# Optimization experiments

Measured on AMD Instinct MI355X. Metric: run time of the kernel, lower is better.

Reference implementation:

```python
import jax, jax.numpy as jnp
import numpy as np

B, T, E, H = 8, 2048, 1024, 64

def setup_inputs() -> dict:
    key = jax.random.key(0)
    kx, kq, kk, kv = jax.random.split(key, 4)
    x = jax.random.normal(kx, (B, T, E), dtype=jnp.float32)
    # torch Linear(E, H, bias=False): weight [H, E]; store transposed [E, H]
    scale = 1.0 / np.sqrt(E)
    Wq = jax.random.uniform(kq, (E, H), dtype=jnp.float32, minval=-scale, maxval=scale)
    Wk = jax.random.uniform(kk, (E, H), dtype=jnp.float32, minval=-scale, maxval=scale)
    Wv = jax.random.uniform(kv, (E, H), dtype=jnp.float32, minval=-scale, maxval=scale)
    return {"x": x, "Wq": Wq, "Wk": Wk, "Wv": Wv}

def reference(x, Wq, Wk, Wv):
    # x: [B,T,E]
    q = x @ Wq  # [B,T,H]
    k = x @ Wk
    v = x @ Wv
    head_size = q.shape[-1]
    scores = jnp.einsum('bth,bsh->bts', q, k) * (head_size ** -0.5)  # [B,T,T]
    Tlen = x.shape[1]
    causal = jnp.tril(jnp.ones((Tlen, Tlen), dtype=bool))
    scores = jnp.where(causal, scores, -jnp.inf)
    weights = jax.nn.softmax(scores, axis=-1)
    # dropout p=0.0 -> identity
    out = jnp.einsum('bts,bsh->bth', weights, v)  # [B,T,H]
    return out
```

## Files before the change

kernel.cpp:

```cpp
#include <hip/hip_runtime.h>
#include <hip/hip_bf16.h>

#define B_  8
#define T_  2048
#define E_  1024
#define H_  64
#define BT_ (B_*T_)

typedef __attribute__((ext_vector_type(8))) __bf16 bf16x8;
typedef __attribute__((ext_vector_type(4))) float  f32x4;

__device__ __forceinline__ unsigned short f2bfu(float f) {
    union { float f; unsigned u; } v; v.f = f;
    unsigned r = v.u + 0x7fffu + ((v.u >> 16) & 1u);
    return (unsigned short)(r >> 16);
}

__device__ __forceinline__ unsigned pk2(float lo, float hi) {
    __hip_bfloat162 h = __float22bfloat162_rn(float2{lo, hi});
    union { __hip_bfloat162 h; unsigned u; } v; v.h = h;
    return v.u;
}

#if defined(__has_builtin)
#if __has_builtin(__builtin_amdgcn_global_load_lds)
#define HAVE_GLL 1
#endif
#endif
__device__ __forceinline__ void dma16(const void* g, void* lds_base, int lane) {
#ifdef HAVE_GLL
    __builtin_amdgcn_global_load_lds(
        (const __attribute__((address_space(1))) unsigned*)(unsigned long long)g,
        (__attribute__((address_space(3))) unsigned*)(unsigned)(unsigned long long)lds_base,
        16, 0, 0);
#else
    *(uint4*)((char*)lds_base + lane * 16) = *(const uint4*)g;
#endif
}

#define QSCALE (0.125f * 1.44269504f)

#define WF_CHUNK_BYTES 12288

__global__ __launch_bounds__(256)
void wprep_kernel(const float* __restrict__ Wq,
                  const float* __restrict__ Wk,
                  const float* __restrict__ Wv,
                  unsigned short* __restrict__ wf)
{
    const int c = blockIdx.x / 3;
    const int m = blockIdx.x % 3;
    const float* W = (m == 0) ? Wq : (m == 1 ? Wk : Wv);
    const float scale = (m == 0) ? QSCALE : 1.0f;

    const int n    = threadIdx.x >> 6;
    const int lane = threadIdx.x & 63;
    const int quad = lane >> 4;
    const int col  = lane & 15;
    const int h    = n * 16 + col;

    unsigned short tmp[8];
#pragma unroll
    for (int j = 0; j < 8; ++j)
        tmp[j] = f2bfu(W[(c * 32 + quad * 8 + j) * H_ + h] * scale);
    *(uint4*)&wf[(((c * 3 + m) * 4 + n) * 64 + lane) * 8] = *(uint4*)tmp;
}

__global__ __launch_bounds__(256, 4)
void qkv_kernel(const float* __restrict__ x,
                const unsigned short* __restrict__ wf,
                unsigned short* __restrict__ qb,
                unsigned short* __restrict__ kb,
                unsigned short* __restrict__ vtb)
{
    __shared__ __align__(16) char  wfs[2][WF_CHUNK_BYTES];
    __shared__ __align__(16) float xs[2][512];

    const int tid  = threadIdx.x;
    const int w    = tid >> 6;
    const int lane = tid & 63;
    const int quad = lane >> 4;
    const int col  = lane & 15;
    const long r0  = (long)blockIdx.x * 16;

    f32x4 acc[3];
#pragma unroll
    for (int m = 0; m < 3; ++m) acc[m] = (f32x4){0.f, 0.f, 0.f, 0.f};

    const char* wfb = (const char*)wf;

    const float* xg = x + (r0 + w * 8 + (lane >> 3)) * E_ + (((lane & 7) ^ (lane >> 3)) * 4);

    const int s0 = (2 * quad) ^ (col & 7);
    const int s1 = s0 ^ 1;

#pragma unroll
    for (int j = 0; j < 3; ++j)
        dma16(wfb + (w * 3 + j) * 1024 + lane * 16, &wfs[0][(w * 3 + j) * 1024], lane);
    if (w < 2) dma16(xg, &xs[0][w * 256], lane);

    for (int c = 0; c < 32; ++c) {
        const int buf = c & 1;
        __syncthreads();

        if (c + 1 < 32) {
#pragma unroll
            for (int j = 0; j < 3; ++j)
                dma16(wfb + (long)(c + 1) * WF_CHUNK_BYTES + (w * 3 + j) * 1024 + lane * 16,
                      &wfs[buf ^ 1][(w * 3 + j) * 1024], lane);
            if (w < 2) dma16(xg + (c + 1) * 32, &xs[buf ^ 1][w * 256], lane);
        }

        float4 f0 = *(const float4*)&xs[buf][col * 32 + s0 * 4];
        float4 f1 = *(const float4*)&xs[buf][col * 32 + s1 * 4];
        unsigned pk[4];
        pk[0] = pk2(f0.x, f0.y);
        pk[1] = pk2(f0.z, f0.w);
        pk[2] = pk2(f1.x, f1.y);
        pk[3] = pk2(f1.z, f1.w);
        bf16x8 af = *(bf16x8*)pk;

#pragma unroll
        for (int m = 0; m < 3; ++m) {
            bf16x8 bm = *(const bf16x8*)&wfs[buf][m * 4096 + w * 1024 + lane * 16];
            acc[m] = __builtin_amdgcn_mfma_f32_16x16x32_bf16(af, bm, acc[m], 0, 0, 0);
        }
    }

    const int bidx = (int)(r0 >> 11);
    const int h    = w * 16 + col;
#pragma unroll
    for (int r = 0; r < 4; ++r) {
        long t = r0 + quad * 4 + r;
        qb[t * H_ + h] = f2bfu(acc[0][r]);
        kb[t * H_ + h] = f2bfu(acc[1][r]);
        vtb[((long)(bidx * H_ + h)) * T_ + (t & (T_ - 1))] = f2bfu(acc[2][r]);
    }
}

#define PSS 72

__global__ __launch_bounds__(512, 2)
void attn_kernel(const unsigned short* __restrict__ qb,
                 const unsigned short* __restrict__ kb,
                 const unsigned short* __restrict__ vtb,
                 float* __restrict__ out)
{
    __shared__ char smem[8 * 16 * 68 * 4 + 8 * 2 * 16 * 4];
    unsigned short* ps = (unsigned short*)smem;
    float* oc = (float*)smem;
    float* ml = (float*)(smem + 8 * 16 * 68 * 4);

    const int tid  = threadIdx.x;
    const int g    = tid >> 6;
    const int lane = tid & 63;
    const int quad = lane >> 4;
    const int col  = lane & 15;
    const int b    = blockIdx.x & 7;
    const int p    = blockIdx.x >> 3;

    const unsigned short* qbb = qb  + (long)b * T_ * H_;
    const unsigned short* kbb = kb  + (long)b * T_ * H_;
    const unsigned short* vbb = vtb + (long)b * H_ * T_;

    for (int half = 0; half < 2; ++half) {
        const int qt = half ? (127 - p) : p;
        const int nt = (qt + 4) >> 2;

        bf16x8 qa0 = *(const bf16x8*)&qbb[(qt * 16 + col) * H_ + quad * 8];
        bf16x8 qa1 = *(const bf16x8*)&qbb[(qt * 16 + col) * H_ + 32 + quad * 8];

        f32x4 o[4];
        float m_i[4], l_i[4];
#pragma unroll
        for (int n = 0; n < 4; ++n) o[n] = (f32x4){0.f, 0.f, 0.f, 0.f};
#pragma unroll
        for (int r = 0; r < 4; ++r) { m_i[r] = -1e30f; l_i[r] = 0.f; }

        bf16x8 kf[8];
        if (g < nt) {
#pragma unroll
            for (int kt = 0; kt < 4; ++kt) {
                const unsigned short* kp = kbb + ((long)(g * 64 + kt * 16 + col)) * H_ + quad * 8;
                kf[kt * 2]     = *(const bf16x8*)kp;
                kf[kt * 2 + 1] = *(const bf16x8*)(kp + 32);
            }
        }

        for (int s = g; s < nt; s += 8) {
            f32x4 sa[4];
#pragma unroll
            for (int kt = 0; kt < 4; ++kt) {
                sa[kt] = (f32x4){0.f, 0.f, 0.f, 0.f};
                sa[kt] = __builtin_amdgcn_mfma_f32_16x16x32_bf16(qa0, kf[kt * 2],     sa[kt], 0, 0, 0);
                sa[kt] = __builtin_amdgcn_mfma_f32_16x16x32_bf16(qa1, kf[kt * 2 + 1], sa[kt], 0, 0, 0);
            }

            bf16x8 vf[8];
#pragma unroll
            for (int n = 0; n < 4; ++n) {
                const unsigned short* vp = vbb + ((long)(n * 16 + col)) * T_ + s * 64 + quad * 8;
                vf[n * 2]     = *(const bf16x8*)vp;
                vf[n * 2 + 1] = *(const bf16x8*)(vp + 32);
            }

            if (s + 8 < nt) {
#pragma unroll
                for (int kt = 0; kt < 4; ++kt) {
                    const unsigned short* kp = kbb + ((long)((s + 8) * 64 + kt * 16 + col)) * H_ + quad * 8;
                    kf[kt * 2]     = *(const bf16x8*)kp;
                    kf[kt * 2 + 1] = *(const bf16x8*)(kp + 32);
                }
            }

            if (s == nt - 1) {
#pragma unroll
                for (int kt = 0; kt < 4; ++kt) {
                    int kg = s * 64 + kt * 16 + col;
#pragma unroll
                    for (int r = 0; r < 4; ++r) {
                        int qg = qt * 16 + quad * 4 + r;
                        if (kg > qg) sa[kt][r] = -1e30f;
                    }
                }
            }

            float mx[4];
#pragma unroll
            for (int r = 0; r < 4; ++r)
                mx[r] = fmaxf(fmaxf(sa[0][r], sa[1][r]), fmaxf(sa[2][r], sa[3][r]));
#pragma unroll
            for (int off = 1; off < 16; off <<= 1)
#pragma unroll
                for (int r = 0; r < 4; ++r)
                    mx[r] = fmaxf(mx[r], __shfl_xor(mx[r], off, 64));

            float alpha[4], mnew[4];
#pragma unroll
            for (int r = 0; r < 4; ++r) {
                mnew[r]  = fmaxf(m_i[r], mx[r]);
                alpha[r] = __builtin_amdgcn_exp2f(m_i[r] - mnew[r]);
                m_i[r]   = mnew[r];
            }

            float rs[4] = {0.f, 0.f, 0.f, 0.f};
#pragma unroll
            for (int kt = 0; kt < 4; ++kt)
#pragma unroll
                for (int r = 0; r < 4; ++r) {
                    float pv = __builtin_amdgcn_exp2f(sa[kt][r] - mnew[r]);
                    rs[r] += pv;
                    ps[g * 16 * PSS + (quad * 4 + r) * PSS + kt * 16 + col] = f2bfu(pv);
                }
#pragma unroll
            for (int off = 1; off < 16; off <<= 1)
#pragma unroll
                for (int r = 0; r < 4; ++r)
                    rs[r] += __shfl_xor(rs[r], off, 64);
#pragma unroll
            for (int r = 0; r < 4; ++r)
                l_i[r] = l_i[r] * alpha[r] + rs[r];

#pragma unroll
            for (int n = 0; n < 4; ++n)
#pragma unroll
                for (int r = 0; r < 4; ++r)
                    o[n][r] *= alpha[r];

            bf16x8 pa0 = *(const bf16x8*)&ps[g * 16 * PSS + col * PSS + quad * 8];
            bf16x8 pa1 = *(const bf16x8*)&ps[g * 16 * PSS + col * PSS + 32 + quad * 8];
#pragma unroll
            for (int n = 0; n < 4; ++n) {
                o[n] = __builtin_amdgcn_mfma_f32_16x16x32_bf16(pa0, vf[n * 2],     o[n], 0, 0, 0);
                o[n] = __builtin_amdgcn_mfma_f32_16x16x32_bf16(pa1, vf[n * 2 + 1], o[n], 0, 0, 0);
            }
        }

        __syncthreads();
#pragma unroll
        for (int r = 0; r < 4; ++r) {
            int row = quad * 4 + r;
#pragma unroll
            for (int n = 0; n < 4; ++n)
                oc[(g * 16 + row) * 68 + n * 16 + col] = o[n][r];
        }
        if (col == 0) {
#pragma unroll
            for (int r = 0; r < 4; ++r) {
                ml[(g * 2 + 0) * 16 + quad * 4 + r] = m_i[r];
                ml[(g * 2 + 1) * 16 + quad * 4 + r] = l_i[r];
            }
        }
        __syncthreads();

#pragma unroll
        for (int rr = 0; rr < 2; ++rr) {
            int row = g * 2 + rr;
            float M = ml[0 * 32 + row];
#pragma unroll
            for (int j = 1; j < 8; ++j) M = fmaxf(M, ml[j * 32 + row]);
            float lsum = 0.f, osum = 0.f;
#pragma unroll
            for (int j = 0; j < 8; ++j) {
                float wgt = __builtin_amdgcn_exp2f(ml[j * 32 + row] - M);
                lsum += ml[j * 32 + 16 + row] * wgt;
                osum += oc[(j * 16 + row) * 68 + lane] * wgt;
            }
            out[((long)b * T_ + qt * 16 + row) * H_ + lane] = osum / lsum;
        }
        __syncthreads();
    }
}

extern "C" void kernel_launch(void* const* d_in, const int* in_sizes, int n_in,
                              void* d_out, int out_size, void* d_ws, size_t ws_size,
                              hipStream_t stream) {
    (void)in_sizes; (void)n_in; (void)out_size; (void)ws_size;
    const float* x  = (const float*)d_in[0];
    const float* Wq = (const float*)d_in[1];
    const float* Wk = (const float*)d_in[2];
    const float* Wv = (const float*)d_in[3];

    unsigned short* qb  = (unsigned short*)d_ws;
    unsigned short* kb  = qb + (size_t)BT_ * H_;
    unsigned short* vtb = kb + (size_t)BT_ * H_;
    unsigned short* wf  = vtb + (size_t)BT_ * H_;

    wprep_kernel<<<96, 256, 0, stream>>>(Wq, Wk, Wv, wf);
    qkv_kernel<<<BT_ / 16, 256, 0, stream>>>(x, wf, qb, kb, vtb);
    attn_kernel<<<B_ * 64, 512, 0, stream>>>(qb, kb, vtb, (float*)d_out);
}
```

Before: 159.8 us.

## Fuse weight prep, QKV projection and attention into one persistent kernel

Replaces three kernel launches with a single persistent kernel of 256 blocks that runs the weight repack, the QKV projection and causal attention in sequence. The phases are separated by software grid barriers built on atomic counters, which are reset with a memset before launch. This removes launch gaps and kernel boundaries. In exchange the grid shrinks from 1024 and 512 blocks to 256 blocks that each do multiple work units, which lowers parallelism and load balancing. The barriers also rely on all blocks being co-resident and add their own spin-wait cost.

Result: slower. 259.4 us (+62.3%).

```diff
diff --git a/kernel.cpp b/kernel.cpp
--- a/kernel.cpp
+++ b/kernel.cpp
@@ -6,6 +6,7 @@
 #define E_  1024
 #define H_  64
 #define BT_ (B_*T_)
+#define NBLK 256
 
 typedef __attribute__((ext_vector_type(8))) __bf16 bf16x8;
 typedef __attribute__((ext_vector_type(4))) float  f32x4;
@@ -38,277 +39,297 @@
 #endif
 }
 
+__device__ __forceinline__ void gridbar(unsigned* cnt, unsigned expected) {
+    __syncthreads();
+    if (threadIdx.x == 0) {
+        __threadfence();
+        __hip_atomic_fetch_add(cnt, 1u, __ATOMIC_RELEASE, __HIP_MEMORY_SCOPE_AGENT);
+        while (__hip_atomic_load(cnt, __ATOMIC_ACQUIRE, __HIP_MEMORY_SCOPE_AGENT) < expected)
+            __builtin_amdgcn_s_sleep(2);
+        __threadfence();
+    }
+    __syncthreads();
+}
+
 #define QSCALE (0.125f * 1.44269504f)
-
 #define WF_CHUNK_BYTES 12288
-
-__global__ __launch_bounds__(256)
-void wprep_kernel(const float* __restrict__ Wq,
+#define PSS 72
+
+__global__ __launch_bounds__(512, 2)
+void fused_kernel(const float* __restrict__ x,
+                  const float* __restrict__ Wq,
                   const float* __restrict__ Wk,
                   const float* __restrict__ Wv,
-                  unsigned short* __restrict__ wf)
+                  unsigned short* __restrict__ qb,
+                  unsigned short* __restrict__ kb,
+                  unsigned short* __restrict__ vtb,
+                  unsigned short* __restrict__ wf,
+                  float* __restrict__ out,
+                  unsigned* __restrict__ bar)
 {
-    const int c = blockIdx.x / 3;
-    const int m = blockIdx.x % 3;
-    const float* W = (m == 0) ? Wq : (m == 1 ? Wk : Wv);
-    const float scale = (m == 0) ? QSCALE : 1.0f;
-
-    const int n    = threadIdx.x >> 6;
-    const int lane = threadIdx.x & 63;
-    const int quad = lane >> 4;
-    const int col  = lane & 15;
-    const int h    = n * 16 + col;
-
-    unsigned short tmp[8];
-#pragma unroll
-    for (int j = 0; j < 8; ++j)
-        tmp[j] = f2bfu(W[(c * 32 + quad * 8 + j) * H_ + h] * scale);
-    *(uint4*)&wf[(((c * 3 + m) * 4 + n) * 64 + lane) * 8] = *(uint4*)tmp;
-}
-
-__global__ __launch_bounds__(256, 4)
-void qkv_kernel(const float* __restrict__ x,
-                const unsigned short* __restrict__ wf,
-                unsigned short* __restrict__ qb,
-                unsigned short* __restrict__ kb,
-                unsigned short* __restrict__ vtb)
-{
-    __shared__ __align__(16) char  wfs[2][WF_CHUNK_BYTES];
-    __shared__ __align__(16) float xs[2][512];
-
-    const int tid  = threadIdx.x;
-    const int w    = tid >> 6;
-    const int lane = tid & 63;
-    const int quad = lane >> 4;
-    const int col  = lane & 15;
-    const long r0  = (long)blockIdx.x * 16;
-
-    f32x4 acc[3];
-#pragma unroll
-    for (int m = 0; m < 3; ++m) acc[m] = (f32x4){0.f, 0.f, 0.f, 0.f};
-
-    const char* wfb = (const char*)wf;
-
-    const float* xg = x + (r0 + w * 8 + (lane >> 3)) * E_ + (((lane & 7) ^ (lane >> 3)) * 4);
-
-    const int s0 = (2 * quad) ^ (col & 7);
-    const int s1 = s0 ^ 1;
-
-#pragma unroll
-    for (int j = 0; j < 3; ++j)
-        dma16(wfb + (w * 3 + j) * 1024 + lane * 16, &wfs[0][(w * 3 + j) * 1024], lane);
-    if (w < 2) dma16(xg, &xs[0][w * 256], lane);
-
-    for (int c = 0; c < 32; ++c) {
-        const int buf = c & 1;
-        __syncthreads();
-
-        if (c + 1 < 32) {
-#pragma unroll
-            for (int j = 0; j < 3; ++j)
-                dma16(wfb + (long)(c + 1) * WF_CHUNK_BYTES + (w * 3 + j) * 1024 + lane * 16,
-                      &wfs[buf ^ 1][(w * 3 + j) * 1024], lane);
-            if (w < 2) dma16(xg + (c + 1) * 32, &xs[buf ^ 1][w * 256], lane);
-        }
-
-        float4 f0 = *(const float4*)&xs[buf][col * 32 + s0 * 4];
-        float4 f1 = *(const float4*)&xs[buf][col * 32 + s1 * 4];
-        unsigned pk[4];
-        pk[0] = pk2(f0.x, f0.y);
-        pk[1] = pk2(f0.z, f0.w);
-        pk[2] = pk2(f1.x, f1.y);
-        pk[3] = pk2(f1.z, f1.w);
-        bf16x8 af = *(bf16x8*)pk;
-
-#pragma unroll
-        for (int m = 0; m < 3; ++m) {
-            bf16x8 bm = *(const bf16x8*)&wfs[buf][m * 4096 + w * 1024 + lane * 16];
-            acc[m] = __builtin_amdgcn_mfma_f32_16x16x32_bf16(af, bm, acc[m], 0, 0, 0);
+    __shared__ __align__(16) char smem[35840];
+    const int tid = threadIdx.x;
+
+    {
+        const int t = blockIdx.x * 512 + tid;
+        if (t < 96 * 256) {
+            const int vb = t >> 8;
+            const int vt = t & 255;
+            const int c = vb / 3;
+            const int m = vb % 3;
+            const float* W = (m == 0) ? Wq : (m == 1 ? Wk : Wv);
+            const float scale = (m == 0) ? QSCALE : 1.0f;
+            const int n    = vt >> 6;
+            const int lane = vt & 63;
+            const int quad = lane >> 4;
+            const int col  = lane & 15;
+            const int h    = n * 16 + col;
+            unsigned short tmp[8];
+#pragma unroll
+            for (int j = 0; j < 8; ++j)
+                tmp[j] = f2bfu(W[(c * 32 + quad * 8 + j) * H_ + h] * scale);
+            *(uint4*)&wf[(((c * 3 + m) * 4 + n) * 64 + lane) * 8] = *(uint4*)tmp;
         }
     }
-
-    const int bidx = (int)(r0 >> 11);
-    const int h    = w * 16 + col;
-#pragma unroll
-    for (int r = 0; r < 4; ++r) {
-        long t = r0 + quad * 4 + r;
-        qb[t * H_ + h] = f2bfu(acc[0][r]);
-        kb[t * H_ + h] = f2bfu(acc[1][r]);
-        vtb[((long)(bidx * H_ + h)) * T_ + (t & (T_ - 1))] = f2bfu(acc[2][r]);
-    }
-}
-
-#define PSS 72
-
-__global__ __launch_bounds__(512, 2)
-void attn_kernel(const unsigned short* __restrict__ qb,
-                 const unsigned short* __restrict__ kb,
-                 const unsigned short* __restrict__ vtb,
-                 float* __restrict__ out)
-{
-    __shared__ char smem[8 * 16 * 68 * 4 + 8 * 2 * 16 * 4];
-    unsigned short* ps = (unsigned short*)smem;
-    float* oc = (float*)smem;
-    float* ml = (float*)(smem + 8 * 16 * 68 * 4);
-
-    const int tid  = threadIdx.x;
-    const int g    = tid >> 6;
-    const int lane = tid & 63;
-    const int quad = lane >> 4;
-    const int col  = lane & 15;
-    const int b    = blockIdx.x & 7;
-    const int p    = blockIdx.x >> 3;
-
-    const unsigned short* qbb = qb  + (long)b * T_ * H_;
-    const unsigned short* kbb = kb  + (long)b * T_ * H_;
-    const unsigned short* vbb = vtb + (long)b * H_ * T_;
-
-    for (int half = 0; half < 2; ++half) {
-        const int qt = half ? (127 - p) : p;
-        const int nt = (qt + 4) >> 2;
-
-        bf16x8 qa0 = *(const bf16x8*)&qbb[(qt * 16 + col) * H_ + quad * 8];
-        bf16x8 qa1 = *(const bf16x8*)&qbb[(qt * 16 + col) * H_ + 32 + quad * 8];
-
-        f32x4 o[4];
-        float m_i[4], l_i[4];
-#pragma unroll
-        for (int n = 0; n < 4; ++n) o[n] = (f32x4){0.f, 0.f, 0.f, 0.f};
-#pragma unroll
-        for (int r = 0; r < 4; ++r) { m_i[r] = -1e30f; l_i[r] = 0.f; }
-
-        bf16x8 kf[8];
-        if (g < nt) {
-#pragma unroll
-            for (int kt = 0; kt < 4; ++kt) {
-                const unsigned short* kp = kbb + ((long)(g * 64 + kt * 16 + col)) * H_ + quad * 8;
-                kf[kt * 2]     = *(const bf16x8*)kp;
-                kf[kt * 2 + 1] = *(const bf16x8*)(kp + 32);
+    gridbar(&bar[0], NBLK);
+
+    {
+        char*  wfs = smem;
+        float* xsb = (float*)(smem + 24576);
+        const int w8   = tid >> 6;
+        const int a    = w8 >> 2;
+        const int wa   = w8 & 3;
+        const int lane = tid & 63;
+        const int quad = lane >> 4;
+        const int col  = lane & 15;
+        const char* wfb = (const char*)wf;
+        const int s0 = (2 * quad) ^ (col & 7);
+        const int s1 = s0 ^ 1;
+        float* xs = xsb + a * 1024;
+
+        for (int pass = 0; pass < 2; ++pass) {
+            const long r0 = ((long)blockIdx.x * 2 + a + pass * 512) * 16;
+            const float* xg = x + (r0 + wa * 8 + (lane >> 3)) * E_
+                                + (((lane & 7) ^ (lane >> 3)) * 4);
+
+            f32x4 acc[3];
+#pragma unroll
+            for (int m = 0; m < 3; ++m) acc[m] = (f32x4){0.f, 0.f, 0.f, 0.f};
+
+            dma16(wfb + w8 * 1024 + lane * 16, &wfs[w8 * 1024], lane);
+            if (w8 < 4)
+                dma16(wfb + (8 + w8) * 1024 + lane * 16, &wfs[(8 + w8) * 1024], lane);
+            if (wa < 2) dma16(xg, &xs[wa * 256], lane);
+
+            for (int c = 0; c < 32; ++c) {
+                const int buf = c & 1;
+                __syncthreads();
+
+                if (c + 1 < 32) {
+                    const char* src = wfb + (long)(c + 1) * WF_CHUNK_BYTES;
+                    char* dst = &wfs[(buf ^ 1) * 12288];
+                    dma16(src + w8 * 1024 + lane * 16, dst + w8 * 1024, lane);
+                    if (w8 < 4)
+                        dma16(src + (8 + w8) * 1024 + lane * 16, dst + (8 + w8) * 1024, lane);
+                    if (wa < 2) dma16(xg + (c + 1) * 32, &xs[(buf ^ 1) * 512 + wa * 256], lane);
+                }
+
+                float4 f0 = *(const float4*)&xs[buf * 512 + col * 32 + s0 * 4];
+                float4 f1 = *(const float4*)&xs[buf * 512 + col * 32 + s1 * 4];
+                unsigned pk[4];
+                pk[0] = pk2(f0.x, f0.y);
+                pk[1] = pk2(f0.z, f0.w);
+                pk[2] = pk2(f1.x, f1.y);
+                pk[3] = pk2(f1.z, f1.w);
+                bf16x8 af = *(bf16x8*)pk;
+
+#pragma unroll
+                for (int m = 0; m < 3; ++m) {
+                    bf16x8 bm = *(const bf16x8*)&wfs[buf * 12288 + m * 4096 + wa * 1024 + lane * 16];
+                    acc[m] = __builtin_amdgcn_mfma_f32_16x16x32_bf16(af, bm, acc[m], 0, 0, 0);
+                }
+            }
+
+            const int bidx = (int)(r0 >> 11);
+            const int h    = wa * 16 + col;
+#pragma unroll
+            for (int r = 0; r < 4; ++r) {
+                long t = r0 + quad * 4 + r;
+                qb[t * H_ + h] = f2bfu(acc[0][r]);
+                kb[t * H_ + h] = f2bfu(acc[1][r]);
+                vtb[((long)(bidx * H_ + h)) * T_ + (t & (T_ - 1))] = f2bfu(acc[2][r]);
             }
         }
-
-        for (int s = g; s < nt; s += 8) {
-            f32x4 sa[4];
-#pragma unroll
-            for (int kt = 0; kt < 4; ++kt) {
-                sa[kt] = (f32x4){0.f, 0.f, 0.f, 0.f};
-                sa[kt] = __builtin_amdgcn_mfma_f32_16x16x32_bf16(qa0, kf[kt * 2],     sa[kt], 0, 0, 0);
-                sa[kt] = __builtin_amdgcn_mfma_f32_16x16x32_bf16(qa1, kf[kt * 2 + 1], sa[kt], 0, 0, 0);
-            }
-
-            bf16x8 vf[8];
-#pragma unroll
-            for (int n = 0; n < 4; ++n) {
-                const unsigned short* vp = vbb + ((long)(n * 16 + col)) * T_ + s * 64 + quad * 8;
-                vf[n * 2]     = *(const bf16x8*)vp;
-                vf[n * 2 + 1] = *(const bf16x8*)(vp + 32);
-            }
-
-            if (s + 8 < nt) {
-#pragma unroll
-                for (int kt = 0; kt < 4; ++kt) {
-                    const unsigned short* kp = kbb + ((long)((s + 8) * 64 + kt * 16 + col)) * H_ + quad * 8;
-                    kf[kt * 2]     = *(const bf16x8*)kp;
-                    kf[kt * 2 + 1] = *(const bf16x8*)(kp + 32);
-                }
-            }
-
-            if (s == nt - 1) {
-#pragma unroll
-                for (int kt = 0; kt < 4; ++kt) {
-                    int kg = s * 64 + kt * 16 + col;
+    }
+    gridbar(&bar[1], NBLK);
+
+    {
+        unsigned short* ps = (unsigned short*)smem;
+        float* oc = (float*)smem;
+        float* ml = (float*)(smem + 8 * 16 * 68 * 4);
+
+        const int g    = tid >> 6;
+        const int lane = tid & 63;
+        const int quad = lane >> 4;
+        const int col  = lane & 15;
+
+        for (int u = 0; u < 2; ++u) {
+            const int unit = blockIdx.x + u * NBLK;
+            const int b = unit & 7;
+            const int p = unit >> 3;
+
+            const unsigned short* qbb = qb  + (long)b * T_ * H_;
+            const unsigned short* kbb = kb  + (long)b * T_ * H_;
+            const unsigned short* vbb = vtb + (long)b * H_ * T_;
+
+            for (int half = 0; half < 2; ++half) {
+                const int qt = half ? (127 - p) : p;
+                const int nt = (qt + 4) >> 2;
+
+                bf16x8 qa0 = *(const bf16x8*)&qbb[(qt * 16 + col) * H_ + quad * 8];
+                bf16x8 qa1 = *(const bf16x8*)&qbb[(qt * 16 + col) * H_ + 32 + quad * 8];
+
+                f32x4 o[4];
+                float m_i[4], l_i[4];
+#pragma unroll
+                for (int n = 0; n < 4; ++n) o[n] = (f32x4){0.f, 0.f, 0.f, 0.f};
+#pragma unroll
+                for (int r = 0; r < 4; ++r) { m_i[r] = -1e30f; l_i[r] = 0.f; }
+
+                bf16x8 kf[8];
+                if (g < nt) {
+#pragma unroll
+                    for (int kt = 0; kt < 4; ++kt) {
+                        const unsigned short* kp = kbb + ((long)(g * 64 + kt * 16 + col)) * H_ + quad * 8;
+                        kf[kt * 2]     = *(const bf16x8*)kp;
+                        kf[kt * 2 + 1] = *(const bf16x8*)(kp + 32);
+                    }
+                }
+
+                for (int s = g; s < nt; s += 8) {
+                    f32x4 sa[4];
+#pragma unroll
+                    for (int kt = 0; kt < 4; ++kt) {
+                        sa[kt] = (f32x4){0.f, 0.f, 0.f, 0.f};
+                        sa[kt] = __builtin_amdgcn_mfma_f32_16x16x32_bf16(qa0, kf[kt * 2],     sa[kt], 0, 0, 0);
+                        sa[kt] = __builtin_amdgcn_mfma_f32_16x16x32_bf16(qa1, kf[kt * 2 + 1], sa[kt], 0, 0, 0);
+                    }
+
+                    bf16x8 vf[8];
+#pragma unroll
+                    for (int n = 0; n < 4; ++n) {
+                        const unsigned short* vp = vbb + ((long)(n * 16 + col)) * T_ + s * 64 + quad * 8;
+                        vf[n * 2]     = *(const bf16x8*)vp;
+                        vf[n * 2 + 1] = *(const bf16x8*)(vp + 32);
+                    }
+
+                    if (s + 8 < nt) {
+#pragma unroll
+                        for (int kt = 0; kt < 4; ++kt) {
+                            const unsigned short* kp = kbb + ((long)((s + 8) * 64 + kt * 16 + col)) * H_ + quad * 8;
+                            kf[kt * 2]     = *(const bf16x8*)kp;
+                            kf[kt * 2 + 1] = *(const bf16x8*)(kp + 32);
+                        }
+                    }
+
+                    if (s == nt - 1) {
+#pragma unroll
+                        for (int kt = 0; kt < 4; ++kt) {
+                            int kg = s * 64 + kt * 16 + col;
+#pragma unroll
+                            for (int r = 0; r < 4; ++r) {
+                                int qg = qt * 16 + quad * 4 + r;
+                                if (kg > qg) sa[kt][r] = -1e30f;
+                            }
+                        }
+                    }
+
+                    float mx[4];
+#pragma unroll
+                    for (int r = 0; r < 4; ++r)
+                        mx[r] = fmaxf(fmaxf(sa[0][r], sa[1][r]), fmaxf(sa[2][r], sa[3][r]));
+#pragma unroll
+                    for (int off = 1; off < 16; off <<= 1)
+#pragma unroll
+                        for (int r = 0; r < 4; ++r)
+                            mx[r] = fmaxf(mx[r], __shfl_xor(mx[r], off, 64));
+
+                    float alpha[4], mnew[4];
 #pragma unroll
                     for (int r = 0; r < 4; ++r) {
-                        int qg = qt * 16 + quad * 4 + r;
-                        if (kg > qg) sa[kt][r] = -1e30f;
-                    }
-                }
-            }
-
-            float mx[4];
-#pragma unroll
-            for (int r = 0; r < 4; ++r)
-                mx[r] = fmaxf(fmaxf(sa[0][r], sa[1][r]), fmaxf(sa[2][r], sa[3][r]));
-#pragma unroll
-            for (int off = 1; off < 16; off <<= 1)
-#pragma unroll
-                for (int r = 0; r < 4; ++r)
-                    mx[r] = fmaxf(mx[r], __shfl_xor(mx[r], off, 64));
-
-            float alpha[4], mnew[4];
-#pragma unroll
-            for (int r = 0; r < 4; ++r) {
-                mnew[r]  = fmaxf(m_i[r], mx[r]);
-                alpha[r] = __builtin_amdgcn_exp2f(m_i[r] - mnew[r]);
-                m_i[r]   = mnew[r];
-            }
-
-            float rs[4] = {0.f, 0.f, 0.f, 0.f};
-#pragma unroll
-            for (int kt = 0; kt < 4; ++kt)
+                        mnew[r]  = fmaxf(m_i[r], mx[r]);
+                        alpha[r] = __builtin_amdgcn_exp2f(m_i[r] - mnew[r]);
+                        m_i[r]   = mnew[r];
+                    }
+
+                    float rs[4] = {0.f, 0.f, 0.f, 0.f};
+#pragma unroll
+                    for (int kt = 0; kt < 4; ++kt)
+#pragma unroll
+                        for (int r = 0; r < 4; ++r) {
+                            float pv = __builtin_amdgcn_exp2f(sa[kt][r] - mnew[r]);
+                            rs[r] += pv;
+                            ps[g * 16 * PSS + (quad * 4 + r) * PSS + kt * 16 + col] = f2bfu(pv);
+                        }
+#pragma unroll
+                    for (int off = 1; off < 16; off <<= 1)
+#pragma unroll
+                        for (int r = 0; r < 4; ++r)
+                            rs[r] += __shfl_xor(rs[r], off, 64);
+#pragma unroll
+                    for (int r = 0; r < 4; ++r)
+                        l_i[r] = l_i[r] * alpha[r] + rs[r];
+
+#pragma unroll
+                    for (int n = 0; n < 4; ++n)
+#pragma unroll
+                        for (int r = 0; r < 4; ++r)
+                            o[n][r] *= alpha[r];
+
+                    bf16x8 pa0 = *(const bf16x8*)&ps[g * 16 * PSS + col * PSS + quad * 8];
+                    bf16x8 pa1 = *(const bf16x8*)&ps[g * 16 * PSS + col * PSS + 32 + quad * 8];
+#pragma unroll
+                    for (int n = 0; n < 4; ++n) {
+                        o[n] = __builtin_amdgcn_mfma_f32_16x16x32_bf16(pa0, vf[n * 2],     o[n], 0, 0, 0);
+                        o[n] = __builtin_amdgcn_mfma_f32_16x16x32_bf16(pa1, vf[n * 2 + 1], o[n], 0, 0, 0);
+                    }
+                }
+
+                __syncthreads();
 #pragma unroll
                 for (int r = 0; r < 4; ++r) {
-                    float pv = __builtin_amdgcn_exp2f(sa[kt][r] - mnew[r]);
-                    rs[r] += pv;
-                    ps[g * 16 * PSS + (quad * 4 + r) * PSS + kt * 16 + col] = f2bfu(pv);
-                }
-#pragma unroll
-            for (int off = 1; off < 16; off <<= 1)
-#pragma unroll
-                for (int r = 0; r < 4; ++r)
-                    rs[r] += __shfl_xor(rs[r], off, 64);
-#pragma unroll
-            for (int r = 0; r < 4; ++r)
-                l_i[r] = l_i[r] * alpha[r] + rs[r];
-
-#pragma unroll
-            for (int n = 0; n < 4; ++n)
-#pragma unroll
-                for (int r = 0; r < 4; ++r)
-                    o[n][r] *= alpha[r];
-
-            bf16x8 pa0 = *(const bf16x8*)&ps[g * 16 * PSS + col * PSS + quad * 8];
-            bf16x8 pa1 = *(const bf16x8*)&ps[g * 16 * PSS + col * PSS + 32 + quad * 8];
-#pragma unroll
-            for (int n = 0; n < 4; ++n) {
-                o[n] = __builtin_amdgcn_mfma_f32_16x16x32_bf16(pa0, vf[n * 2],     o[n], 0, 0, 0);
-                o[n] = __builtin_amdgcn_mfma_f32_16x16x32_bf16(pa1, vf[n * 2 + 1], o[n], 0, 0, 0);
+                    int row = quad * 4 + r;
+#pragma unroll
+                    for (int n = 0; n < 4; ++n)
+                        oc[(g * 16 + row) * 68 + n * 16 + col] = o[n][r];
+                }
+                if (col == 0) {
+#pragma unroll
+                    for (int r = 0; r < 4; ++r) {
+                        ml[(g * 2 + 0) * 16 + quad * 4 + r] = m_i[r];
+                        ml[(g * 2 + 1) * 16 + quad * 4 + r] = l_i[r];
+                    }
+                }
+                __syncthreads();
+
+#pragma unroll
+                for (int rr = 0; rr < 2; ++rr) {
+                    int row = g * 2 + rr;
+                    float M = ml[0 * 32 + row];
+#pragma unroll
+                    for (int j = 1; j < 8; ++j) M = fmaxf(M, ml[j * 32 + row]);
+                    float lsum = 0.f, osum = 0.f;
+#pragma unroll
+                    for (int j = 0; j < 8; ++j) {
+                        float wgt = __builtin_amdgcn_exp2f(ml[j * 32 + row] - M);
+                        lsum += ml[j * 32 + 16 + row] * wgt;
+                        osum += oc[(j * 16 + row) * 68 + lane] * wgt;
+                    }
+                    out[((long)b * T_ + qt * 16 + row) * H_ + lane] = osum / lsum;
+                }
+                __syncthreads();
             }
         }
-
-        __syncthreads();
-#pragma unroll
-        for (int r = 0; r < 4; ++r) {
-            int row = quad * 4 + r;
-#pragma unroll
-            for (int n = 0; n < 4; ++n)
-                oc[(g * 16 + row) * 68 + n * 16 + col] = o[n][r];
-        }
-        if (col == 0) {
-#pragma unroll
-            for (int r = 0; r < 4; ++r) {
-                ml[(g * 2 + 0) * 16 + quad * 4 + r] = m_i[r];
-                ml[(g * 2 + 1) * 16 + quad * 4 + r] = l_i[r];
-            }
-        }
-        __syncthreads();
-
-#pragma unroll
-        for (int rr = 0; rr < 2; ++rr) {
-            int row = g * 2 + rr;
-            float M = ml[0 * 32 + row];
-#pragma unroll
-            for (int j = 1; j < 8; ++j) M = fmaxf(M, ml[j * 32 + row]);
-            float lsum = 0.f, osum = 0.f;
-#pragma unroll
-            for (int j = 0; j < 8; ++j) {
-                float wgt = __builtin_amdgcn_exp2f(ml[j * 32 + row] - M);
-                lsum += ml[j * 32 + 16 + row] * wgt;
-                osum += oc[(j * 16 + row) * 68 + lane] * wgt;
-            }
-            out[((long)b * T_ + qt * 16 + row) * H_ + lane] = osum / lsum;
-        }
-        __syncthreads();
     }
 }
 
@@ -325,8 +346,9 @@
     unsigned short* kb  = qb + (size_t)BT_ * H_;
     unsigned short* vtb = kb + (size_t)BT_ * H_;
     unsigned short* wf  = vtb + (size_t)BT_ * H_;
-
-    wprep_kernel<<<96, 256, 0, stream>>>(Wq, Wk, Wv, wf);
-    qkv_kernel<<<BT_ / 16, 256, 0, stream>>>(x, wf, qb, kb, vtb);
-    attn_kernel<<<B_ * 64, 512, 0, stream>>>(qb, kb, vtb, (float*)d_out);
-}
+    unsigned*       bar = (unsigned*)(wf + (size_t)3 * H_ * E_);
+    float*          out = (float*)d_out;
+
+    hipMemsetAsync(bar, 0, 64, stream);
+    fused_kernel<<<NBLK, 512, 0, stream>>>(x, Wq, Wk, Wv, qb, kb, vtb, wf, out, bar);
+}
```
